# Optimization experiments

Measured on AMD Instinct MI355X. Metric: run time of the kernel, lower is better.

## Reference

```python
import itertools
import jax, jax.numpy as jnp
import numpy as np

GRID = (41, 1600, 1408)   # KITTI voxel grid (z, y, x)
N_VOX = 80000
C_IN, C_OUT = 32, 64
NEG_SLOPE = 0.01          # nn.LeakyReLU default
BN_EPS = 1e-5

# ---------- numpy rulebook construction (spconv indice pairs) ----------

def _lin(c, grid):
    return (c[:, 0] * grid[1] + c[:, 1]) * grid[2] + c[:, 2]

def _lookup(lin_sorted, q, valid):
    pos = np.searchsorted(lin_sorted, q)
    pos = np.clip(pos, 0, len(lin_sorted) - 1)
    found = valid & (lin_sorted[pos] == q)
    return np.where(found, pos, len(lin_sorted)).astype(np.int32)  # sentinel = N

def _offsets(kshape, d):
    rs = [([-d, 0, d] if s == 3 else [0]) for s in kshape]
    return list(itertools.product(*rs))

def _subm_map(coords, lin_sorted, grid, kshape, d):
    offs = _offsets(kshape, d)
    g = np.asarray(grid)
    nbr = np.empty((len(offs), len(coords)), np.int32)
    for k, off in enumerate(offs):
        q = coords + np.asarray(off)
        valid = ((q >= 0) & (q < g)).all(1)
        nbr[k] = _lookup(lin_sorted, _lin(q, grid), valid)
    return nbr

def _build_maps(seed=0):
    rng = np.random.default_rng(seed)
    tot = GRID[0] * GRID[1] * GRID[2]
    lin0 = np.sort(rng.choice(tot, size=N_VOX, replace=False))
    c0 = np.stack(np.unravel_index(lin0, GRID), axis=1).astype(np.int64)
    nbr331_d1 = _subm_map(c0, lin0, GRID, (3, 3, 1), 1)
    nbr313_d1 = _subm_map(c0, lin0, GRID, (3, 1, 3), 1)
    # SparseConv3d k=3 s=2 p=1: output active sites = union over inputs/offsets
    og = tuple((g + 2 - 3) // 2 + 1 for g in GRID)
    offs27 = np.asarray(list(itertools.product(range(3), repeat=3)))
    cand = c0[None, :, :] + 1 - offs27[:, None, :]
    ok = (cand % 2 == 0).all(-1)
    p = cand // 2
    ok &= ((p >= 0) & (p < np.asarray(og))).all(-1)
    plin = (p[..., 0] * og[1] + p[..., 1]) * og[2] + p[..., 2]
    lin1 = np.unique(plin[ok])
    c1 = np.stack(np.unravel_index(lin1, og), axis=1).astype(np.int64)
    M = len(c1)
    pool_nbr = np.empty((27, M), np.int32)
    gg = np.asarray(GRID)
    for k in range(27):
        q = c1 * 2 - 1 + offs27[k]
        valid = ((q >= 0) & (q < gg)).all(1)
        pool_nbr[k] = _lookup(lin0, _lin(q, GRID), valid)
    nbr331_d2 = _subm_map(c1, lin1, og, (3, 3, 1), 2)
    nbr313_d2 = _subm_map(c1, lin1, og, (3, 1, 3), 2)
    nbr331_d3 = _subm_map(c1, lin1, og, (3, 3, 1), 3)
    nbr313_d3 = _subm_map(c1, lin1, og, (3, 1, 3), 3)
    maps = dict(nbr331_d1=jnp.asarray(nbr331_d1), nbr313_d1=jnp.asarray(nbr313_d1),
                pool_nbr=jnp.asarray(pool_nbr), nbr331_d2=jnp.asarray(nbr331_d2),
                nbr313_d2=jnp.asarray(nbr313_d2), nbr331_d3=jnp.asarray(nbr331_d3),
                nbr313_d3=jnp.asarray(nbr313_d3))
    return maps, M

# ---------- jax forward ----------

def _subm(f, nbr, W):
    # gather-GEMM-scatter sparse conv: out[n] = sum_k f[nbr[k,n]] @ W[k]
    padf = jnp.concatenate([f, jnp.zeros((1, f.shape[1]), f.dtype)], 0)  # zero row for missing nbr
    out = jnp.zeros((nbr.shape[1], W.shape[2]), f.dtype)
    for k in range(nbr.shape[0]):  # fixed small kernel-volume loop (9 or 27)
        out = out + padf[nbr[k]] @ W[k]
    return out

def _bn_act(x):
    # BatchNorm1d (training stats, gamma=1, beta=0 per weight_initialization) + LeakyReLU
    m = jnp.mean(x, 0)
    v = jnp.var(x, 0)
    return jax.nn.leaky_relu((x - m) * jax.lax.rsqrt(v + BN_EPS), NEG_SLOPE)

def _res(f, nA, nB, w1, w12, w2, w22):
    # nA: (3,3,1) map (conv3x1), nB: (3,1,3) map (conv1x3)
    s = _bn_act(_subm(f, nA, w1))
    s = _bn_act(_subm(s, nB, w12))
    r = _bn_act(_subm(f, nB, w2))
    r = _bn_act(_subm(r, nA, w22))
    return r + s

def setup_inputs() -> dict:
    maps, M = _build_maps()
    ks = jax.random.split(jax.random.key(0), 16)
    def w(k, shape):
        fan = shape[-2] * (shape[0] if len(shape) == 3 else 1)
        return jax.random.normal(k, shape, jnp.float32) / np.sqrt(fan)
    inp = dict(
        feats=jax.random.normal(ks[0], (N_VOX, C_IN), jnp.float32),
        b1_w1=w(ks[1], (9, C_IN, C_OUT)), b1_w1_2=w(ks[2], (9, C_OUT, C_OUT)),
        b1_w2=w(ks[3], (9, C_IN, C_OUT)), b1_w2_2=w(ks[4], (9, C_OUT, C_OUT)),
        pool_w=w(ks[5], (27, C_OUT, C_OUT)),
        b2_w1=w(ks[6], (9, C_OUT, C_OUT)), b2_w1_2=w(ks[7], (9, C_OUT, C_OUT)),
        b2_w2=w(ks[8], (9, C_OUT, C_OUT)), b2_w2_2=w(ks[9], (9, C_OUT, C_OUT)),
        b3_w1=w(ks[10], (9, C_OUT, C_OUT)), b3_w1_2=w(ks[11], (9, C_OUT, C_OUT)),
        b3_w2=w(ks[12], (9, C_OUT, C_OUT)), b3_w2_2=w(ks[13], (9, C_OUT, C_OUT)),
        down_w=w(ks[14], (3 * C_OUT, C_OUT)),
    )
    inp.update(maps)
    return inp

def reference(feats, b1_w1, b1_w1_2, b1_w2, b1_w2_2, pool_w,
              b2_w1, b2_w1_2, b2_w2, b2_w2_2,
              b3_w1, b3_w1_2, b3_w2, b3_w2_2, down_w,
              nbr331_d1, nbr313_d1, pool_nbr,
              nbr331_d2, nbr313_d2, nbr331_d3, nbr313_d3):
    x1 = _res(feats, nbr331_d1, nbr313_d1, b1_w1, b1_w1_2, b1_w2, b1_w2_2)
    x1 = _subm(x1, pool_nbr, pool_w)                     # strided SparseConv3d pool -> [M, C]
    x2 = _res(x1, nbr331_d2, nbr313_d2, b2_w1, b2_w1_2, b2_w2, b2_w2_2)  # dilation 2
    x3 = _res(x2, nbr331_d3, nbr313_d3, b3_w1, b3_w1_2, b3_w2, b3_w2_2)  # dilation 3
    return jnp.concatenate([x1, x2, x3], -1) @ down_w     # 1x1 subm conv fuse
```

## Files before the change

### kernel.cpp

```cpp
#include <hip/hip_runtime.h>
#include <hip/hip_bf16.h>

#define NEG 0.01f
#define BN_EPS 1e-5f

typedef __hip_bfloat16 bf16;
typedef __attribute__((ext_vector_type(8))) short short8;
typedef __attribute__((ext_vector_type(16))) float f32x16;

__device__ __forceinline__ float b2f(short s) {
    unsigned u = ((unsigned)(unsigned short)s) << 16;
    float f;
    __builtin_memcpy(&f, &u, 4);
    return f;
}
__device__ __forceinline__ short f2b(float f) {
    union { bf16 b; short s; } t;
    t.b = __float2bfloat16(f);
    return t.s;
}

__global__ void finalize2_k(const float* __restrict__ sA, const float* __restrict__ sB,
                            float* __restrict__ fA, float* __restrict__ fB,
                            float inv_n) {
    const float* s = blockIdx.x == 0 ? sA : sB;
    float* f = blockIdx.x == 0 ? fA : fB;
    int c = threadIdx.x;
    float sm = 0.f, sq = 0.f;
    #pragma unroll
    for (int k = 0; k < 32; ++k) {
        sm += s[k * 256 + c];
        sq += s[k * 256 + 64 + c];
    }
    float m = sm * inv_n;
    float v = sq * inv_n - m * m;
    f[c] = m;
    f[64 + c] = rsqrtf(v + BN_EPS);
}


__global__ __launch_bounds__(256) void bnact2_k(
    bf16* __restrict__ xa, const float* __restrict__ fa,
    bf16* __restrict__ xb, const float* __restrict__ fb, int nvec) {
    int i = blockIdx.x * blockDim.x + threadIdx.x;
    if (i >= 2 * nvec) return;
    bf16* x; const float* f; int j;
    if (i < nvec) { x = xa; f = fa; j = i; }
    else          { x = xb; f = fb; j = i - nvec; }
    const int c0 = (j & 7) << 3;
    short8 v = *reinterpret_cast<const short8*>(x + ((size_t)j << 3));
    short8 o;
    #pragma unroll
    for (int e = 0; e < 8; ++e) {
        float t = (b2f(v[e]) - f[c0 + e]) * f[64 + c0 + e];
        t = t > 0.f ? t : NEG * t;
        o[e] = f2b(t);
    }
    *reinterpret_cast<short8*>(x + ((size_t)j << 3)) = o;
}

__global__ __launch_bounds__(256) void bnadd_k(
    const bf16* __restrict__ a, const float* __restrict__ fa,
    const bf16* __restrict__ b, const float* __restrict__ fb,
    bf16* __restrict__ out, int nvec) {
    int i = blockIdx.x * blockDim.x + threadIdx.x;
    if (i >= nvec) return;
    const int c0 = (i & 7) << 3;
    short8 va = *reinterpret_cast<const short8*>(a + ((size_t)i << 3));
    short8 vb = *reinterpret_cast<const short8*>(b + ((size_t)i << 3));
    short8 o;
    #pragma unroll
    for (int e = 0; e < 8; ++e) {
        float ta = (b2f(va[e]) - fa[c0 + e]) * fa[64 + c0 + e];
        ta = ta > 0.f ? ta : NEG * ta;
        float tb = (b2f(vb[e]) - fb[c0 + e]) * fb[64 + c0 + e];
        tb = tb > 0.f ? tb : NEG * tb;
        o[e] = f2b(ta + tb);
    }
    *reinterpret_cast<short8*>(out + ((size_t)i << 3)) = o;
}

__global__ void cvt_f32_bf16_k(const float* __restrict__ x, bf16* __restrict__ y, int n) {
    int i = blockIdx.x * blockDim.x + threadIdx.x;
    if (i < n) y[i] = __float2bfloat16(x[i]);
}

struct PackEnt { const float* src; bf16* dst; int kt; int ns; };
struct PackArgs { PackEnt e[16]; };

__global__ void pack_w_k(PackArgs pa) {
    PackEnt E = pa.e[blockIdx.y];
    int cin = E.ns * 16;
    int total = E.kt * E.ns * 1024;
    for (int i = blockIdx.x * blockDim.x + threadIdx.x; i < total;
         i += gridDim.x * blockDim.x) {
        int j = i & 7, lane = (i >> 3) & 63, c = (i >> 9) & 1;
        int rem = i >> 10;
        int s = rem % E.ns, k = rem / E.ns;
        int krow = s * 16 + ((lane >> 5) << 3) + j;
        int col = c * 32 + (lane & 31);
        E.dst[i] = __float2bfloat16(E.src[((size_t)k * cin + krow) * 64 + col]);
    }
}

struct Job {
    const bf16* fin; const int* nbr; const bf16* Wp; bf16* out; float* stat;
    int n_out, n_in;
};
struct Jobs4 { Job j[2]; int b_split; };

template <int NS, int K>
__global__ __launch_bounds__(512, 4) void mconv4(Jobs4 jb) {
    __shared__ short8 WL[K * NS * 128];
    const int CIN = NS * 16;
    const int tid = threadIdx.x;
    const int lane = tid & 63;
    const int col = lane & 31;
    const int q = lane >> 5;
    const int widl = tid >> 6;
    const int nwl = blockDim.x >> 6;

    const int nb = gridDim.x;
    const int qq = nb >> 3, rr = nb & 7;
    const int xcd = blockIdx.x & 7, bi = blockIdx.x >> 3;
    const int sb = (xcd < rr) ? xcd * (qq + 1) + bi
                              : rr * (qq + 1) + (xcd - rr) * qq + bi;

    const int jsel = (sb >= jb.b_split) ? 1 : 0;
    const Job J = jb.j[jsel];
    const int lb = jsel ? sb - jb.b_split : sb;
    const int nbj = jsel ? nb - jb.b_split : jb.b_split;
    const int ntiles = (J.n_out + 31) >> 5;

    {
        const short8* wsrc = (const short8*)J.Wp;
        for (int i = tid; i < K * NS * 128; i += blockDim.x) WL[i] = wsrc[i];
    }
    __syncthreads();

    const int wid = lb * nwl + widl;
    const int nw = nbj * nwl;

    for (int tile = wid; tile < ntiles; tile += nw) {
        const int rbase = tile << 5;
        const int r = rbase + col;
        const bool rowok = r < J.n_out;

        f32x16 acc0, acc1;
        #pragma unroll
        for (int i = 0; i < 16; ++i) { acc0[i] = 0.f; acc1[i] = 0.f; }

        int idx[K];
        #pragma unroll
        for (int t = 0; t < K; ++t)
            idx[t] = rowok ? J.nbr[(size_t)t * J.n_out + r] : J.n_in;

        auto loadA = [&](int id, short8 (&dst)[NS]) {
            const bool v = id < J.n_in;
            const bf16* src = J.fin + (size_t)id * CIN + q * 8;
            #pragma unroll
            for (int s = 0; s < NS; ++s) {
                short8 z = {0, 0, 0, 0, 0, 0, 0, 0};
                dst[s] = z;
                if (v) dst[s] = *(const short8*)(src + s * 16);
            }
        };
        auto dotap = [&](int k, int id, short8 (&a)[NS]) {
            if (__ballot(id < J.n_in) == 0ull) return;
            #pragma unroll
            for (int s = 0; s < NS; ++s) {
                short8 b0 = WL[((k * NS + s) * 2 + 0) * 64 + lane];
                short8 b1 = WL[((k * NS + s) * 2 + 1) * 64 + lane];
                acc0 = __builtin_amdgcn_mfma_f32_32x32x16_bf16(a[s], b0, acc0, 0, 0, 0);
                acc1 = __builtin_amdgcn_mfma_f32_32x32x16_bf16(a[s], b1, acc1, 0, 0, 0);
            }
        };

        short8 A0[NS], A1[NS];
        loadA(idx[0], A0);
        #pragma unroll 1
        for (int t = 0; t + 2 <= K; t += 2) {
            loadA(idx[t + 1], A1);
            dotap(t, idx[t], A0);
            if (t + 2 < K) loadA(idx[t + 2], A0);
            dotap(t + 1, idx[t + 1], A1);
        }
        dotap(K - 1, idx[K - 1], A0);

        float s0 = 0.f, q0 = 0.f, s1 = 0.f, q1 = 0.f;
        #pragma unroll
        for (int i = 0; i < 16; ++i) {
            int row = (i & 3) + 8 * (i >> 2) + 4 * q;
            int gr = rbase + row;
            if (gr < J.n_out) {
                float v0 = acc0[i], v1 = acc1[i];
                J.out[(size_t)gr * 64 + col] = __float2bfloat16(v0);
                J.out[(size_t)gr * 64 + 32 + col] = __float2bfloat16(v1);
                s0 += v0; q0 += v0 * v0;
                s1 += v1; q1 += v1 * v1;
            }
        }
        if (J.stat != nullptr) {
            s0 += __shfl_xor(s0, 32); q0 += __shfl_xor(q0, 32);
            s1 += __shfl_xor(s1, 32); q1 += __shfl_xor(q1, 32);
            float* st = J.stat + (((sb << 3) + widl) & 31) * 256;
            if (q == 0) {
                atomicAdd(&st[col], s0);
                atomicAdd(&st[64 + col], q0);
            } else {
                atomicAdd(&st[32 + col], s1);
                atomicAdd(&st[96 + col], q1);
            }
        }
    }
}

template <int NS>
__global__ __launch_bounds__(512, 4) void mpool_k(
    const bf16* __restrict__ fin, const int* __restrict__ nbr,
    const bf16* __restrict__ Wp, bf16* __restrict__ out,
    int n_out, int n_in) {
    __shared__ short8 WL[9 * NS * 128];
    const int CIN = NS * 16;
    const int tid = threadIdx.x;
    const int lane = tid & 63;
    const int col = lane & 31;
    const int q = lane >> 5;
    const int widl = tid >> 6;

    const int nb = gridDim.x;
    const int qq = nb >> 3, rr = nb & 7;
    const int xcd = blockIdx.x & 7, bi = blockIdx.x >> 3;
    const int sb = (xcd < rr) ? xcd * (qq + 1) + bi
                              : rr * (qq + 1) + (xcd - rr) * qq + bi;

    const int ntiles = (n_out + 31) >> 5;
    const int nbatch = (ntiles + 7) >> 3;

    for (int batch = sb; batch < nbatch; batch += nb) {
        const int tile = (batch << 3) + widl;
        const int rbase = tile << 5;
        const int r = rbase + col;
        const bool rowok = (tile < ntiles) && (r < n_out);

        f32x16 acc0, acc1;
        #pragma unroll
        for (int i = 0; i < 16; ++i) { acc0[i] = 0.f; acc1[i] = 0.f; }

        auto loadA = [&](int id, short8 (&dst)[NS]) {
            const bool v = id < n_in;
            const bf16* src = fin + (size_t)id * CIN + q * 8;
            #pragma unroll
            for (int s = 0; s < NS; ++s) {
                short8 z = {0, 0, 0, 0, 0, 0, 0, 0};
                dst[s] = z;
                if (v) dst[s] = *(const short8*)(src + s * 16);
            }
        };
        auto dotap = [&](int k, int id, short8 (&a)[NS]) {
            if (__ballot(id < n_in) == 0ull) return;
            #pragma unroll
            for (int s = 0; s < NS; ++s) {
                short8 b0 = WL[((k * NS + s) * 2 + 0) * 64 + lane];
                short8 b1 = WL[((k * NS + s) * 2 + 1) * 64 + lane];
                acc0 = __builtin_amdgcn_mfma_f32_32x32x16_bf16(a[s], b0, acc0, 0, 0, 0);
                acc1 = __builtin_amdgcn_mfma_f32_32x32x16_bf16(a[s], b1, acc1, 0, 0, 0);
            }
        };

        #pragma unroll 1
        for (int g = 0; g < 3; ++g) {
            __syncthreads();
            {
                const short8* wsrc = (const short8*)Wp + (size_t)g * (9 * NS * 128);
                #pragma unroll
                for (int i = 0; i < (9 * NS * 128) / 512; ++i)
                    WL[i * 512 + tid] = wsrc[i * 512 + tid];
            }
            __syncthreads();

            int idx[9];
            #pragma unroll
            for (int t = 0; t < 9; ++t)
                idx[t] = rowok ? nbr[(size_t)(g * 9 + t) * n_out + r] : n_in;

            short8 A0[NS], A1[NS];
            loadA(idx[0], A0);
            #pragma unroll 1
            for (int t = 0; t + 2 <= 9; t += 2) {
                loadA(idx[t + 1], A1);
                dotap(t, idx[t], A0);
                if (t + 2 < 9) loadA(idx[t + 2], A0);
                dotap(t + 1, idx[t + 1], A1);
            }
            dotap(8, idx[8], A0);
        }

        #pragma unroll
        for (int i = 0; i < 16; ++i) {
            int row = (i & 3) + 8 * (i >> 2) + 4 * q;
            int gr = rbase + row;
            if (tile < ntiles && gr < n_out) {
                out[(size_t)gr * 64 + col] = __float2bfloat16(acc0[i]);
                out[(size_t)gr * 64 + 32 + col] = __float2bfloat16(acc1[i]);
            }
        }
    }
}

__global__ __launch_bounds__(256, 6) void down_k(
    const bf16* __restrict__ x1, const bf16* __restrict__ x2,
    const bf16* __restrict__ x3, const bf16* __restrict__ W1,
    const bf16* __restrict__ W2, const bf16* __restrict__ W3,
    float* __restrict__ out, int m) {
    const int lane = threadIdx.x & 63;
    const int col = lane & 31;
    const int q = lane >> 5;
    const int wid = blockIdx.x * (blockDim.x >> 6) + (threadIdx.x >> 6);
    const int nw = gridDim.x * (blockDim.x >> 6);
    const int ntiles = (m + 31) >> 5;

    for (int tile = wid; tile < ntiles; tile += nw) {
        const int rbase = tile << 5;
        const int r = rbase + col;
        const bool rowok = r < m;

        f32x16 acc0, acc1;
        #pragma unroll
        for (int i = 0; i < 16; ++i) { acc0[i] = 0.f; acc1[i] = 0.f; }

        const bf16* xs[3] = {x1, x2, x3};
        const bf16* ws[3] = {W1, W2, W3};
        #pragma unroll 1
        for (int t = 0; t < 3; ++t) {
            const bf16* src = xs[t] + (size_t)r * 64 + q * 8;
            const short8* wp = (const short8*)ws[t] + lane;
            #pragma unroll
            for (int s = 0; s < 4; ++s) {
                short8 a;
                if (rowok) a = *(const short8*)(src + s * 16);
                else { short8 z = {0,0,0,0,0,0,0,0}; a = z; }
                short8 b0 = wp[(s * 2 + 0) * 64];
                short8 b1 = wp[(s * 2 + 1) * 64];
                acc0 = __builtin_amdgcn_mfma_f32_32x32x16_bf16(a, b0, acc0, 0, 0, 0);
                acc1 = __builtin_amdgcn_mfma_f32_32x32x16_bf16(a, b1, acc1, 0, 0, 0);
            }
        }
        #pragma unroll
        for (int i = 0; i < 16; ++i) {
            int row = (i & 3) + 8 * (i >> 2) + 4 * q;
            int gr = rbase + row;
            if (gr < m) {
                out[(size_t)gr * 64 + col] = acc0[i];
                out[(size_t)gr * 64 + 32 + col] = acc1[i];
            }
        }
    }
}


extern "C" void kernel_launch(void* const* d_in, const int* in_sizes, int n_in_,
                              void* d_out, int out_size, void* d_ws,
                              size_t ws_size, hipStream_t stream) {
    const float* feats = (const float*)d_in[0];
    const float* Wsrc[16] = {
        (const float*)d_in[1], (const float*)d_in[2],
        (const float*)d_in[3], (const float*)d_in[4],
        (const float*)d_in[5],
        (const float*)d_in[6], (const float*)d_in[7],
        (const float*)d_in[8], (const float*)d_in[9],
        (const float*)d_in[10], (const float*)d_in[11],
        (const float*)d_in[12], (const float*)d_in[13],
        (const float*)d_in[14],
        (const float*)d_in[14] + 64 * 64,
        (const float*)d_in[14] + 128 * 64,
    };
    const int kts[16] = {9,9,9,9, 27, 9,9,9,9, 9,9,9,9, 1,1,1};
    const int nss[16] = {2,4,2,4,  4, 4,4,4,4, 4,4,4,4, 4,4,4};

    const int* nA1 = (const int*)d_in[15];
    const int* nB1 = (const int*)d_in[16];
    const int* pnbr = (const int*)d_in[17];
    const int* nA2 = (const int*)d_in[18];
    const int* nB2 = (const int*)d_in[19];
    const int* nA3 = (const int*)d_in[20];
    const int* nB3 = (const int*)d_in[21];

    const int N = in_sizes[0] / 32;
    const int M = in_sizes[17] / 27;
    const size_t MX = (size_t)(N > M ? N : M);

    bf16* A = (bf16*)d_ws;
    bf16* B = A + MX * 64;
    bf16* C = B + MX * 64;
    bf16* D = C + MX * 64;
    bf16* E = D + MX * 64;
    bf16* FB = E + MX * 64;
    bf16* WP = FB + (size_t)N * 32;
    bf16* G = (bf16*)d_out;
    bf16* Wp[16];
    {
        size_t off = 0;
        for (int i = 0; i < 16; ++i) {
            Wp[i] = WP + off;
            off += (size_t)kts[i] * nss[i] * 1024;
        }
    }
    size_t wp_total = 0;
    for (int i = 0; i < 16; ++i) wp_total += (size_t)kts[i] * nss[i] * 1024;
    float* ST = (float*)(WP + wp_total + (wp_total & 1));
    float* FS = ST + (size_t)12 * 32 * 256;
    float* out = (float*)d_out;
    auto S = [&](int i) { return ST + (size_t)i * 32 * 256; };
    auto F = [&](int i) { return FS + (size_t)i * 128; };

    hipMemsetAsync(ST, 0, (size_t)12 * 32 * 256 * sizeof(float), stream);
    {
        PackArgs pa;
        for (int i = 0; i < 16; ++i) pa.e[i] = {Wsrc[i], Wp[i], kts[i], nss[i]};
        pack_w_k<<<dim3(64, 16), 256, 0, stream>>>(pa);
    }
    cvt_f32_bf16_k<<<(N * 32 + 255) / 256, 256, 0, stream>>>(feats, FB, N * 32);

    const float invN = 1.f / (float)N, invM = 1.f / (float)M;
    const int nvN = N * 8, nvM = M * 8;

    auto mkjob = [](const bf16* fin, const int* nbr, const bf16* w, bf16* o,
                    float* st, int no, int ni) {
        Job j; j.fin = fin; j.nbr = nbr; j.Wp = w; j.out = o; j.stat = st;
        j.n_out = no; j.n_in = ni; return j;
    };
    auto pair4 = [&](void (*kp)(Jobs4), Job a, Job b) {
        Jobs4 jb; jb.j[0] = a; jb.j[1] = b;
        const int nb = 512;
        long ta = (a.n_out + 31) >> 5, tb = (b.n_out + 31) >> 5;
        int bs = (int)((ta * nb + (ta + tb) / 2) / (ta + tb));
        if (bs < 1) bs = 1;
        if (bs > nb - 1) bs = nb - 1;
        jb.b_split = bs;
        hipLaunchKernelGGL(kp, dim3(nb), dim3(512), 0, stream, jb);
    };

    pair4(mconv4<2, 9>,
          mkjob(FB, nA1, Wp[0], A, S(0), N, N),
          mkjob(FB, nB1, Wp[2], B, S(2), N, N));
    finalize2_k<<<2, 64, 0, stream>>>(S(0), S(2), F(0), F(2), invN);
    bnact2_k<<<(2 * nvN + 255) / 256, 256, 0, stream>>>(A, F(0), B, F(2), nvN);
    pair4(mconv4<4, 9>,
          mkjob(A, nB1, Wp[1], C, S(1), N, N),
          mkjob(B, nA1, Wp[3], E, S(3), N, N));
    finalize2_k<<<2, 64, 0, stream>>>(S(1), S(3), F(1), F(3), invN);
    bnadd_k<<<(nvN + 255) / 256, 256, 0, stream>>>(C, F(1), E, F(3), B, nvN);

    mpool_k<4><<<512, 512, 0, stream>>>(B, pnbr, Wp[4], D, M, N);

    pair4(mconv4<4, 9>,
          mkjob(D, nA2, Wp[5], A, S(4), M, M),
          mkjob(D, nB2, Wp[7], B, S(6), M, M));
    finalize2_k<<<2, 64, 0, stream>>>(S(4), S(6), F(4), F(6), invM);
    bnact2_k<<<(2 * nvM + 255) / 256, 256, 0, stream>>>(A, F(4), B, F(6), nvM);
    pair4(mconv4<4, 9>,
          mkjob(A, nB2, Wp[6], C, S(5), M, M),
          mkjob(B, nA2, Wp[8], E, S(7), M, M));
    finalize2_k<<<2, 64, 0, stream>>>(S(5), S(7), F(5), F(7), invM);
    bnadd_k<<<(nvM + 255) / 256, 256, 0, stream>>>(C, F(5), E, F(7), E, nvM);

    pair4(mconv4<4, 9>,
          mkjob(E, nA3, Wp[9], A, S(8), M, M),
          mkjob(E, nB3, Wp[11], B, S(10), M, M));
    finalize2_k<<<2, 64, 0, stream>>>(S(8), S(10), F(8), F(10), invM);
    bnact2_k<<<(2 * nvM + 255) / 256, 256, 0, stream>>>(A, F(8), B, F(10), nvM);
    pair4(mconv4<4, 9>,
          mkjob(A, nB3, Wp[10], C, S(9), M, M),
          mkjob(B, nA3, Wp[12], G, S(11), M, M));
    finalize2_k<<<2, 64, 0, stream>>>(S(9), S(11), F(9), F(11), invM);
    bnadd_k<<<(nvM + 255) / 256, 256, 0, stream>>>(C, F(9), G, F(11), B, nvM);

    {
        int blocks = (((M + 31) >> 5) + 3) >> 2;
        down_k<<<blocks, 256, 0, stream>>>(D, E, B, Wp[13], Wp[14], Wp[15], out, M);
    }
}
```

Measured before the change: 602.6 us.

## Stage row-coalesced neighbor gathers through swizzled LDS in sparse conv kernels

The conv and pool kernels change how they gather neighbor feature rows. Before, each lane loaded strided 16-byte pieces of its own row in MFMA operand layout. Now the lanes of a wave shuffle the neighbor indices so that consecutive lanes load contiguous chunks of the same rows. Those chunks are written to a per-wave LDS staging buffer with an XOR swizzle and read back in MFMA layout. Neighbor indices are now fetched one tap ahead instead of all up front, and launch bounds drop from 4 to 2 blocks per CU to allow more registers. This adds LDS traffic and lowers occupancy, and invalid sentinel rows are now loaded unconditionally and zeroed afterwards.

```diff
diff --git a/kernel.cpp b/kernel.cpp
--- a/kernel.cpp
+++ b/kernel.cpp
@@ -110,8 +110,13 @@
 struct Jobs4 { Job j[2]; int b_split; };
 
 template <int NS, int K>
-__global__ __launch_bounds__(512, 4) void mconv4(Jobs4 jb) {
+__global__ __launch_bounds__(512, 2) void mconv5(Jobs4 jb) {
+    constexpr int CHUNKS = NS * 2;
+    constexpr int CMASK = CHUNKS - 1;
+    constexpr int LOG2C = (NS == 4) ? 3 : 2;
+    constexpr int RPI = 64 / CHUNKS;
     __shared__ short8 WL[K * NS * 128];
+    __shared__ short8 STG[8][32 * CHUNKS];
     const int CIN = NS * 16;
     const int tid = threadIdx.x;
     const int lane = tid & 63;
@@ -150,42 +155,53 @@
         #pragma unroll
         for (int i = 0; i < 16; ++i) { acc0[i] = 0.f; acc1[i] = 0.f; }
 
-        int idx[K];
-        #pragma unroll
-        for (int t = 0; t < K; ++t)
-            idx[t] = rowok ? J.nbr[(size_t)t * J.n_out + r] : J.n_in;
-
-        auto loadA = [&](int id, short8 (&dst)[NS]) {
-            const bool v = id < J.n_in;
-            const bf16* src = J.fin + (size_t)id * CIN + q * 8;
+        short8 G[NS];
+        auto issue = [&](int idxv) {
+            #pragma unroll
+            for (int h = 0; h < NS; ++h) {
+                int rid = __shfl(idxv, h * RPI + (lane >> LOG2C));
+                const bf16* src = J.fin + (size_t)rid * CIN + ((lane & CMASK) << 3);
+                G[h] = *(const short8*)src;
+            }
+        };
+        auto wstage = [&]() {
+            #pragma unroll
+            for (int h = 0; h < NS; ++h) {
+                int rl = h * RPI + (lane >> LOG2C);
+                int slot = (lane & CMASK) ^ (rl & CMASK);
+                STG[widl][rl * CHUNKS + slot] = G[h];
+            }
+        };
+        auto dotap = [&](int t, int idxown) {
+            if (__ballot(idxown < J.n_in) == 0ull) return;
+            const bool v = idxown < J.n_in;
             #pragma unroll
             for (int s = 0; s < NS; ++s) {
-                short8 z = {0, 0, 0, 0, 0, 0, 0, 0};
-                dst[s] = z;
-                if (v) dst[s] = *(const short8*)(src + s * 16);
-            }
-        };
-        auto dotap = [&](int k, int id, short8 (&a)[NS]) {
-            if (__ballot(id < J.n_in) == 0ull) return;
-            #pragma unroll
-            for (int s = 0; s < NS; ++s) {
-                short8 b0 = WL[((k * NS + s) * 2 + 0) * 64 + lane];
-                short8 b1 = WL[((k * NS + s) * 2 + 1) * 64 + lane];
-                acc0 = __builtin_amdgcn_mfma_f32_32x32x16_bf16(a[s], b0, acc0, 0, 0, 0);
-                acc1 = __builtin_amdgcn_mfma_f32_32x32x16_bf16(a[s], b1, acc1, 0, 0, 0);
-            }
-        };
-
-        short8 A0[NS], A1[NS];
-        loadA(idx[0], A0);
+                int slot = (2 * s + q) ^ (lane & CMASK);
+                short8 a = STG[widl][col * CHUNKS + slot];
+                if (!v) { short8 z = {0,0,0,0,0,0,0,0}; a = z; }
+                short8 b0 = WL[((t * NS + s) * 2 + 0) * 64 + lane];
+                short8 b1 = WL[((t * NS + s) * 2 + 1) * 64 + lane];
+                acc0 = __builtin_amdgcn_mfma_f32_32x32x16_bf16(a, b0, acc0, 0, 0, 0);
+                acc1 = __builtin_amdgcn_mfma_f32_32x32x16_bf16(a, b1, acc1, 0, 0, 0);
+            }
+        };
+        auto ldidx = [&](int t) {
+            return rowok ? J.nbr[(size_t)t * J.n_out + r] : J.n_in;
+        };
+
+        int i0 = ldidx(0);
+        issue(i0);
+        int i1 = (K > 1) ? ldidx(1) : J.n_in;
+        wstage();
         #pragma unroll 1
-        for (int t = 0; t + 2 <= K; t += 2) {
-            loadA(idx[t + 1], A1);
-            dotap(t, idx[t], A0);
-            if (t + 2 < K) loadA(idx[t + 2], A0);
-            dotap(t + 1, idx[t + 1], A1);
-        }
-        dotap(K - 1, idx[K - 1], A0);
+        for (int t = 0; t < K; ++t) {
+            if (t + 1 < K) issue(i1);
+            dotap(t, i0);
+            if (t + 1 < K) wstage();
+            int inx = (t + 2 < K) ? ldidx(t + 2) : J.n_in;
+            i0 = i1; i1 = inx;
+        }
 
         float s0 = 0.f, q0 = 0.f, s1 = 0.f, q1 = 0.f;
         #pragma unroll
@@ -216,11 +232,16 @@
 }
 
 template <int NS>
-__global__ __launch_bounds__(512, 4) void mpool_k(
+__global__ __launch_bounds__(512, 2) void mpool2_k(
     const bf16* __restrict__ fin, const int* __restrict__ nbr,
     const bf16* __restrict__ Wp, bf16* __restrict__ out,
     int n_out, int n_in) {
+    constexpr int CHUNKS = NS * 2;
+    constexpr int CMASK = CHUNKS - 1;
+    constexpr int LOG2C = 3;
+    constexpr int RPI = 64 / CHUNKS;
     __shared__ short8 WL[9 * NS * 128];
+    __shared__ short8 STG[8][32 * CHUNKS];
     const int CIN = NS * 16;
     const int tid = threadIdx.x;
     const int lane = tid & 63;
@@ -247,24 +268,35 @@
         #pragma unroll
         for (int i = 0; i < 16; ++i) { acc0[i] = 0.f; acc1[i] = 0.f; }
 
-        auto loadA = [&](int id, short8 (&dst)[NS]) {
-            const bool v = id < n_in;
-            const bf16* src = fin + (size_t)id * CIN + q * 8;
+        short8 G[NS];
+        auto issue = [&](int idxv) {
+            #pragma unroll
+            for (int h = 0; h < NS; ++h) {
+                int rid = __shfl(idxv, h * RPI + (lane >> LOG2C));
+                const bf16* src = fin + (size_t)rid * CIN + ((lane & CMASK) << 3);
+                G[h] = *(const short8*)src;
+            }
+        };
+        auto wstage = [&]() {
+            #pragma unroll
+            for (int h = 0; h < NS; ++h) {
+                int rl = h * RPI + (lane >> LOG2C);
+                int slot = (lane & CMASK) ^ (rl & CMASK);
+                STG[widl][rl * CHUNKS + slot] = G[h];
+            }
+        };
+        auto dotap = [&](int t, int idxown) {
+            if (__ballot(idxown < n_in) == 0ull) return;
+            const bool v = idxown < n_in;
             #pragma unroll
             for (int s = 0; s < NS; ++s) {
-                short8 z = {0, 0, 0, 0, 0, 0, 0, 0};
-                dst[s] = z;
-                if (v) dst[s] = *(const short8*)(src + s * 16);
-            }
-        };
-        auto dotap = [&](int k, int id, short8 (&a)[NS]) {
-            if (__ballot(id < n_in) == 0ull) return;
-            #pragma unroll
-            for (int s = 0; s < NS; ++s) {
-                short8 b0 = WL[((k * NS + s) * 2 + 0) * 64 + lane];
-                short8 b1 = WL[((k * NS + s) * 2 + 1) * 64 + lane];
-                acc0 = __builtin_amdgcn_mfma_f32_32x32x16_bf16(a[s], b0, acc0, 0, 0, 0);
-                acc1 = __builtin_amdgcn_mfma_f32_32x32x16_bf16(a[s], b1, acc1, 0, 0, 0);
+                int slot = (2 * s + q) ^ (lane & CMASK);
+                short8 a = STG[widl][col * CHUNKS + slot];
+                if (!v) { short8 z = {0,0,0,0,0,0,0,0}; a = z; }
+                short8 b0 = WL[((t * NS + s) * 2 + 0) * 64 + lane];
+                short8 b1 = WL[((t * NS + s) * 2 + 1) * 64 + lane];
+                acc0 = __builtin_amdgcn_mfma_f32_32x32x16_bf16(a, b0, acc0, 0, 0, 0);
+                acc1 = __builtin_amdgcn_mfma_f32_32x32x16_bf16(a, b1, acc1, 0, 0, 0);
             }
         };
 
@@ -279,21 +311,21 @@
             }
             __syncthreads();
 
-            int idx[9];
-            #pragma unroll
-            for (int t = 0; t < 9; ++t)
-                idx[t] = rowok ? nbr[(size_t)(g * 9 + t) * n_out + r] : n_in;
-
-            short8 A0[NS], A1[NS];
-            loadA(idx[0], A0);
+            auto ldidx = [&](int t) {
+                return rowok ? nbr[(size_t)(g * 9 + t) * n_out + r] : n_in;
+            };
+            int i0 = ldidx(0);
+            issue(i0);
+            int i1 = ldidx(1);
+            wstage();
             #pragma unroll 1
-            for (int t = 0; t + 2 <= 9; t += 2) {
-                loadA(idx[t + 1], A1);
-                dotap(t, idx[t], A0);
-                if (t + 2 < 9) loadA(idx[t + 2], A0);
-                dotap(t + 1, idx[t + 1], A1);
-            }
-            dotap(8, idx[8], A0);
+            for (int t = 0; t < 9; ++t) {
+                if (t + 1 < 9) issue(i1);
+                dotap(t, i0);
+                if (t + 1 < 9) wstage();
+                int inx = (t + 2 < 9) ? ldidx(t + 2) : n_in;
+                i0 = i1; i1 = inx;
+            }
         }
 
         #pragma unroll
@@ -414,7 +446,7 @@
     auto S = [&](int i) { return ST + (size_t)i * 32 * 256; };
     auto F = [&](int i) { return FS + (size_t)i * 128; };
 
-    hipMemsetAsync(ST, 0, (size_t)12 * 32 * 256 * sizeof(float), stream);
+    (void)hipMemsetAsync(ST, 0, (size_t)12 * 32 * 256 * sizeof(float), stream);
     {
         PackArgs pa;
         for (int i = 0; i < 16; ++i) pa.e[i] = {Wsrc[i], Wp[i], kts[i], nss[i]};
@@ -441,36 +473,36 @@
         hipLaunchKernelGGL(kp, dim3(nb), dim3(512), 0, stream, jb);
     };
 
-    pair4(mconv4<2, 9>,
+    pair4(mconv5<2, 9>,
           mkjob(FB, nA1, Wp[0], A, S(0), N, N),
           mkjob(FB, nB1, Wp[2], B, S(2), N, N));
     finalize2_k<<<2, 64, 0, stream>>>(S(0), S(2), F(0), F(2), invN);
     bnact2_k<<<(2 * nvN + 255) / 256, 256, 0, stream>>>(A, F(0), B, F(2), nvN);
-    pair4(mconv4<4, 9>,
+    pair4(mconv5<4, 9>,
           mkjob(A, nB1, Wp[1], C, S(1), N, N),
           mkjob(B, nA1, Wp[3], E, S(3), N, N));
     finalize2_k<<<2, 64, 0, stream>>>(S(1), S(3), F(1), F(3), invN);
     bnadd_k<<<(nvN + 255) / 256, 256, 0, stream>>>(C, F(1), E, F(3), B, nvN);
 
-    mpool_k<4><<<512, 512, 0, stream>>>(B, pnbr, Wp[4], D, M, N);
-
-    pair4(mconv4<4, 9>,
+    mpool2_k<4><<<512, 512, 0, stream>>>(B, pnbr, Wp[4], D, M, N);
+
+    pair4(mconv5<4, 9>,
           mkjob(D, nA2, Wp[5], A, S(4), M, M),
           mkjob(D, nB2, Wp[7], B, S(6), M, M));
     finalize2_k<<<2, 64, 0, stream>>>(S(4), S(6), F(4), F(6), invM);
     bnact2_k<<<(2 * nvM + 255) / 256, 256, 0, stream>>>(A, F(4), B, F(6), nvM);
-    pair4(mconv4<4, 9>,
+    pair4(mconv5<4, 9>,
           mkjob(A, nB2, Wp[6], C, S(5), M, M),
           mkjob(B, nA2, Wp[8], E, S(7), M, M));
     finalize2_k<<<2, 64, 0, stream>>>(S(5), S(7), F(5), F(7), invM);
     bnadd_k<<<(nvM + 255) / 256, 256, 0, stream>>>(C, F(5), E, F(7), E, nvM);
 
-    pair4(mconv4<4, 9>,
+    pair4(mconv5<4, 9>,
           mkjob(E, nA3, Wp[9], A, S(8), M, M),
           mkjob(E, nB3, Wp[11], B, S(10), M, M));
     finalize2_k<<<2, 64, 0, stream>>>(S(8), S(10), F(8), F(10), invM);
     bnact2_k<<<(2 * nvM + 255) / 256, 256, 0, stream>>>(A, F(8), B, F(10), nvM);
-    pair4(mconv4<4, 9>,
+    pair4(mconv5<4, 9>,
           mkjob(A, nB3, Wp[10], C, S(9), M, M),
           mkjob(B, nA3, Wp[12], G, S(11), M, M));
     finalize2_k<<<2, 64, 0, stream>>>(S(9), S(11), F(9), F(11), invM);
```

Measured after the change: 822.8 us. +36.5%, slower.
